# Performance work log

Measured on AMD Instinct MI355X. Metric: run time of the kernel, lower is better.

The kernel has to match this reference:

```python
import jax, jax.numpy as jnp
import numpy as np

N_ENV, N_STEP = 4096, 2048
GAMMA, LAMBDA = 0.99, 0.95


def setup_inputs() -> dict:
    key = jax.random.key(0)
    k1, k2, k3 = jax.random.split(key, 3)
    rewards = jax.random.normal(k1, (N_ENV, N_STEP), dtype=jnp.float32)
    values = jax.random.normal(k2, (N_ENV, N_STEP + 1), dtype=jnp.float32)
    first = (jax.random.uniform(k3, (N_ENV, N_STEP + 1)) < 0.01).astype(jnp.float32)
    return {"rewards": rewards, "values": values, "first": first}


def reference(rewards, values, first):
    """GAE backward recurrence, vectorized over envs via a reverse lax.scan.

    advantages[t] = delta[t] + notlast[t]*gamma*lambda*advantages[t+1]
    delta[t]      = r[t] + notlast[t]*gamma*V[t+1] - V[t]
    """
    notlast = 1.0 - first[:, 1:]                        # [E, T]
    delta = rewards + notlast * GAMMA * values[:, 1:] - values[:, :-1]  # [E, T]

    def step(lastgaelam, xs):
        d_t, nl_t = xs                                  # each [E]
        adv_t = d_t + nl_t * (GAMMA * LAMBDA) * lastgaelam
        return adv_t, adv_t

    init = jnp.zeros(rewards.shape[0], dtype=rewards.dtype)
    _, advs = jax.lax.scan(step, init, (delta.T, notlast.T), reverse=True)
    advantages = advs.T                                 # [E, T]
    v_targ = values[:, :-1] + advantages
    return advantages, v_targ
```

## Files before the change

### kernel.cpp

```cpp
#include <hip/hip_runtime.h>


constexpr int NE   = 4096;
constexpr int NT   = 2048;
constexpr int NT1  = 2049;
constexpr float GAMMA  = 0.99f;
constexpr float LAMBDA = 0.95f;
constexpr int TPB = 256;
constexpr int PER = NT / TPB;
constexpr int NQ  = NT / 4;
constexpr int QPT = NQ / TPB;

typedef float f32x4 __attribute__((ext_vector_type(4)));
typedef float f32x4u __attribute__((ext_vector_type(4), aligned(4)));

__device__ __forceinline__ f32x4 ld4u(const float* p) {
    return (f32x4)*reinterpret_cast<const f32x4u*>(p);
}

__device__ __forceinline__ int swz(int g) { return g ^ ((g >> 3) & 7); }

__global__ __launch_bounds__(TPB) void gae_kernel(
    const float* __restrict__ rewards,
    const float* __restrict__ values,
    const float* __restrict__ first,
    float* __restrict__ out)
{
    __shared__ f32x4 d_lds[NQ];
    __shared__ f32x4 c_lds[NQ];
    __shared__ float sWA[4];
    __shared__ float sWB[4];

    const int e    = blockIdx.x;
    const int tid  = threadIdx.x;
    const int lane = tid & 63;
    const int w    = tid >> 6;

    const float* r_row = rewards + (size_t)e * NT;
    const float* v_row = values  + (size_t)e * NT1;
    const float* f_row = first   + (size_t)e * NT1;

    f32x4 vreg[QPT];
#pragma unroll
    for (int j = 0; j < QPT; ++j) {
        const int q = j * TPB + tid;
        const int t = 4 * q;
        const f32x4 r4  = *reinterpret_cast<const f32x4*>(r_row + t);
        const f32x4 v4a = ld4u(v_row + t);
        const f32x4 f4  = ld4u(f_row + t + 1);
        float vnext = __shfl_down(v4a.x, 1);
        if (lane == 63) vnext = v_row[t + 4];
        f32x4 v4b; v4b.x = v4a.y; v4b.y = v4a.z; v4b.z = v4a.w; v4b.w = vnext;
        vreg[j] = v4a;
        const f32x4 nl = 1.0f - f4;
        const f32x4 d4 = r4 + nl * GAMMA * v4b - v4a;
        const f32x4 c4 = nl * (GAMMA * LAMBDA);
        d_lds[swz(q)] = d4;
        c_lds[swz(q)] = c4;
    }
    __syncthreads();

    float d[PER], c[PER];
    {
        const f32x4 da = d_lds[swz(2 * tid)];
        const f32x4 db = d_lds[swz(2 * tid + 1)];
        const f32x4 ca = c_lds[swz(2 * tid)];
        const f32x4 cb = c_lds[swz(2 * tid + 1)];
        d[0]=da.x; d[1]=da.y; d[2]=da.z; d[3]=da.w;
        d[4]=db.x; d[5]=db.y; d[6]=db.z; d[7]=db.w;
        c[0]=ca.x; c[1]=ca.y; c[2]=ca.z; c[3]=ca.w;
        c[4]=cb.x; c[5]=cb.y; c[6]=cb.z; c[7]=cb.w;
    }

    float A = 1.0f, B = 0.0f;
#pragma unroll
    for (int k = PER - 1; k >= 0; --k) {
        B = fmaf(c[k], B, d[k]);
        A *= c[k];
    }

    float cA = A, cB = B;
#pragma unroll
    for (int off = 1; off < 64; off <<= 1) {
        const float a2 = __shfl_down(cA, off);
        const float b2 = __shfl_down(cB, off);
        if (lane + off < 64) {
            cB = fmaf(cA, b2, cB);
            cA = cA * a2;
        }
    }

    if (lane == 0) { sWA[w] = cA; sWB[w] = cB; }

    float EA = __shfl_down(cA, 1);
    float EB = __shfl_down(cB, 1);
    if (lane == 63) { EA = 1.0f; EB = 0.0f; }

    __syncthreads();

    float TB = 0.0f;
    for (int u = 3; u > w; --u) {
        TB = fmaf(sWA[u], TB, sWB[u]);
    }
    float x = fmaf(EA, TB, EB);

    float adv[PER];
#pragma unroll
    for (int k = PER - 1; k >= 0; --k) {
        x = fmaf(c[k], x, d[k]);
        adv[k] = x;
    }
    {
        f32x4 a0; a0.x=adv[0]; a0.y=adv[1]; a0.z=adv[2]; a0.w=adv[3];
        f32x4 a1; a1.x=adv[4]; a1.y=adv[5]; a1.z=adv[6]; a1.w=adv[7];
        d_lds[swz(2 * tid)]     = a0;
        d_lds[swz(2 * tid + 1)] = a1;
    }
    __syncthreads();

    float* __restrict__ adv_out = out + (size_t)e * NT;
    float* __restrict__ vt_out  = out + (size_t)NE * NT + (size_t)e * NT;
#pragma unroll
    for (int j = 0; j < QPT; ++j) {
        const int q = j * TPB + tid;
        const int t = 4 * q;
        const f32x4 a4 = d_lds[swz(q)];
        const f32x4 vt = vreg[j] + a4;
        __builtin_nontemporal_store(a4, reinterpret_cast<f32x4*>(adv_out + t));
        __builtin_nontemporal_store(vt, reinterpret_cast<f32x4*>(vt_out + t));
    }
}

extern "C" void kernel_launch(void* const* d_in, const int* in_sizes, int n_in,
                              void* d_out, int out_size, void* d_ws, size_t ws_size,
                              hipStream_t stream) {
    const float* rewards = (const float*)d_in[0];
    const float* values  = (const float*)d_in[1];
    const float* first   = (const float*)d_in[2];
    float* out = (float*)d_out;
    gae_kernel<<<NE, TPB, 0, stream>>>(rewards, values, first, out);
}
```

Measured before the change: 30.29 us.

## Map one wavefront per env row with chunked scan and register prefetch

Each wavefront now owns a whole environment row and walks it backward in 8 chunks of 256 steps, doing a 64-lane shuffle scan per chunk and carrying the running advantage between chunks. This drops the LDS staging, swizzling and block-wide barriers of the one-block-per-row design and launches a quarter as many blocks. Loads are software-pipelined three chunks ahead in registers to hide memory latency. The trade is a serial chain of eight shuffle scans per wave in place of one block-wide scan, which adds shuffle work per element.

```diff
diff --git a/kernel.cpp b/kernel.cpp
--- a/kernel.cpp
+++ b/kernel.cpp
@@ -7,9 +7,7 @@
 constexpr float GAMMA  = 0.99f;
 constexpr float LAMBDA = 0.95f;
 constexpr int TPB = 256;
-constexpr int PER = NT / TPB;
-constexpr int NQ  = NT / 4;
-constexpr int QPT = NQ / TPB;
+constexpr int NG  = NT / 256;
 
 typedef float f32x4 __attribute__((ext_vector_type(4)));
 typedef float f32x4u __attribute__((ext_vector_type(4), aligned(4)));
@@ -18,117 +16,89 @@
     return (f32x4)*reinterpret_cast<const f32x4u*>(p);
 }
 
-__device__ __forceinline__ int swz(int g) { return g ^ ((g >> 3) & 7); }
-
 __global__ __launch_bounds__(TPB) void gae_kernel(
     const float* __restrict__ rewards,
     const float* __restrict__ values,
     const float* __restrict__ first,
     float* __restrict__ out)
 {
-    __shared__ f32x4 d_lds[NQ];
-    __shared__ f32x4 c_lds[NQ];
-    __shared__ float sWA[4];
-    __shared__ float sWB[4];
-
-    const int e    = blockIdx.x;
     const int tid  = threadIdx.x;
     const int lane = tid & 63;
     const int w    = tid >> 6;
+    const int e    = blockIdx.x * 4 + w;
 
     const float* r_row = rewards + (size_t)e * NT;
     const float* v_row = values  + (size_t)e * NT1;
     const float* f_row = first   + (size_t)e * NT1;
+    float* adv_out = out + (size_t)e * NT;
+    float* vt_out  = out + (size_t)NE * NT + (size_t)e * NT;
 
-    f32x4 vreg[QPT];
+    const int l4 = lane * 4;
+
+    f32x4 rb[3], vb[3], fb[3];
+#define LOADG(s, g)                                                     \
+    do {                                                                \
+        const int _t = (g) * 256 + l4;                                  \
+        rb[s] = *reinterpret_cast<const f32x4*>(r_row + _t);            \
+        vb[s] = ld4u(v_row + _t);                                       \
+        fb[s] = ld4u(f_row + _t + 1);                                   \
+    } while (0)
+
+    LOADG(0, 7); LOADG(1, 6); LOADG(2, 5);
+
+    float carry   = 0.0f;
+    float prevTop = v_row[NT];
+
 #pragma unroll
-    for (int j = 0; j < QPT; ++j) {
-        const int q = j * TPB + tid;
-        const int t = 4 * q;
-        const f32x4 r4  = *reinterpret_cast<const f32x4*>(r_row + t);
-        const f32x4 v4a = ld4u(v_row + t);
-        const f32x4 f4  = ld4u(f_row + t + 1);
-        float vnext = __shfl_down(v4a.x, 1);
-        if (lane == 63) vnext = v_row[t + 4];
-        f32x4 v4b; v4b.x = v4a.y; v4b.y = v4a.z; v4b.z = v4a.w; v4b.w = vnext;
-        vreg[j] = v4a;
+    for (int g = NG - 1; g >= 0; --g) {
+        const int s = (NG - 1 - g) % 3;
+        const f32x4 r4 = rb[s];
+        const f32x4 v4 = vb[s];
+        const f32x4 f4 = fb[s];
+        if (g >= 3) LOADG(s, g - 3);
+
+        float vnext = __shfl_down(v4.x, 1);
+        const float top = __shfl(v4.x, 0);
+        if (lane == 63) vnext = prevTop;
+        prevTop = top;
+
         const f32x4 nl = 1.0f - f4;
-        const f32x4 d4 = r4 + nl * GAMMA * v4b - v4a;
+        f32x4 v4b; v4b.x = v4.y; v4b.y = v4.z; v4b.z = v4.w; v4b.w = vnext;
+        const f32x4 d4 = r4 + nl * GAMMA * v4b - v4;
         const f32x4 c4 = nl * (GAMMA * LAMBDA);
-        d_lds[swz(q)] = d4;
-        c_lds[swz(q)] = c4;
-    }
-    __syncthreads();
 
-    float d[PER], c[PER];
-    {
-        const f32x4 da = d_lds[swz(2 * tid)];
-        const f32x4 db = d_lds[swz(2 * tid + 1)];
-        const f32x4 ca = c_lds[swz(2 * tid)];
-        const f32x4 cb = c_lds[swz(2 * tid + 1)];
-        d[0]=da.x; d[1]=da.y; d[2]=da.z; d[3]=da.w;
-        d[4]=db.x; d[5]=db.y; d[6]=db.z; d[7]=db.w;
-        c[0]=ca.x; c[1]=ca.y; c[2]=ca.z; c[3]=ca.w;
-        c[4]=cb.x; c[5]=cb.y; c[6]=cb.z; c[7]=cb.w;
-    }
+        const float B = d4.x + c4.x * (d4.y + c4.y * (d4.z + c4.z * d4.w));
+        const float A = c4.x * c4.y * c4.z * c4.w;
 
-    float A = 1.0f, B = 0.0f;
+        float cA = A, cB = B;
 #pragma unroll
-    for (int k = PER - 1; k >= 0; --k) {
-        B = fmaf(c[k], B, d[k]);
-        A *= c[k];
-    }
+        for (int off = 1; off < 64; off <<= 1) {
+            const float a2 = __shfl_down(cA, off);
+            const float b2 = __shfl_down(cB, off);
+            if (lane + off < 64) {
+                cB = fmaf(cA, b2, cB);
+                cA = cA * a2;
+            }
+        }
+        float EA = __shfl_down(cA, 1);
+        float EB = __shfl_down(cB, 1);
+        if (lane == 63) { EA = 1.0f; EB = 0.0f; }
+        const float newcarry = fmaf(__shfl(cA, 0), carry, __shfl(cB, 0));
+        float x = fmaf(EA, carry, EB);
+        carry = newcarry;
 
-    float cA = A, cB = B;
-#pragma unroll
-    for (int off = 1; off < 64; off <<= 1) {
-        const float a2 = __shfl_down(cA, off);
-        const float b2 = __shfl_down(cB, off);
-        if (lane + off < 64) {
-            cB = fmaf(cA, b2, cB);
-            cA = cA * a2;
-        }
-    }
+        f32x4 a4;
+        x = fmaf(c4.w, x, d4.w); a4.w = x;
+        x = fmaf(c4.z, x, d4.z); a4.z = x;
+        x = fmaf(c4.y, x, d4.y); a4.y = x;
+        x = fmaf(c4.x, x, d4.x); a4.x = x;
+        const f32x4 vt = v4 + a4;
 
-    if (lane == 0) { sWA[w] = cA; sWB[w] = cB; }
-
-    float EA = __shfl_down(cA, 1);
-    float EB = __shfl_down(cB, 1);
-    if (lane == 63) { EA = 1.0f; EB = 0.0f; }
-
-    __syncthreads();
-
-    float TB = 0.0f;
-    for (int u = 3; u > w; --u) {
-        TB = fmaf(sWA[u], TB, sWB[u]);
-    }
-    float x = fmaf(EA, TB, EB);
-
-    float adv[PER];
-#pragma unroll
-    for (int k = PER - 1; k >= 0; --k) {
-        x = fmaf(c[k], x, d[k]);
-        adv[k] = x;
-    }
-    {
-        f32x4 a0; a0.x=adv[0]; a0.y=adv[1]; a0.z=adv[2]; a0.w=adv[3];
-        f32x4 a1; a1.x=adv[4]; a1.y=adv[5]; a1.z=adv[6]; a1.w=adv[7];
-        d_lds[swz(2 * tid)]     = a0;
-        d_lds[swz(2 * tid + 1)] = a1;
-    }
-    __syncthreads();
-
-    float* __restrict__ adv_out = out + (size_t)e * NT;
-    float* __restrict__ vt_out  = out + (size_t)NE * NT + (size_t)e * NT;
-#pragma unroll
-    for (int j = 0; j < QPT; ++j) {
-        const int q = j * TPB + tid;
-        const int t = 4 * q;
-        const f32x4 a4 = d_lds[swz(q)];
-        const f32x4 vt = vreg[j] + a4;
+        const int t = g * 256 + l4;
         __builtin_nontemporal_store(a4, reinterpret_cast<f32x4*>(adv_out + t));
         __builtin_nontemporal_store(vt, reinterpret_cast<f32x4*>(vt_out + t));
     }
+#undef LOADG
 }
 
 extern "C" void kernel_launch(void* const* d_in, const int* in_sizes, int n_in,
@@ -138,5 +108,5 @@
     const float* values  = (const float*)d_in[1];
     const float* first   = (const float*)d_in[2];
     float* out = (float*)d_out;
-    gae_kernel<<<NE, TPB, 0, stream>>>(rewards, values, first, out);
+    gae_kernel<<<NE / 4, TPB, 0, stream>>>(rewards, values, first, out);
 }
```

New measurement: 30.07 us. Within noise of the previous version (-0.7%).
